# Kernel optimization log

Measured on AMD Instinct MI355X. Metric: run time of the kernel, lower is better.

The kernel has to match this reference:

```python
import jax, jax.numpy as jnp
import numpy as np

B, T, F, H = 64, 2048, 256, 512


def setup_inputs() -> dict:
    key = jax.random.key(0)
    ks = jax.random.split(key, 8)
    s_ih = 1.0 / np.sqrt(H)
    return {
        "z": jax.random.normal(ks[0], (B, H), dtype=jnp.float32),
        "x": jax.random.normal(ks[1], (B, T, F), dtype=jnp.float32),
        "W_ih": jax.random.uniform(ks[2], (4 * H, F), minval=-s_ih, maxval=s_ih, dtype=jnp.float32),
        "W_hh": jax.random.uniform(ks[3], (4 * H, H), minval=-s_ih, maxval=s_ih, dtype=jnp.float32),
        "b_ih": jax.random.uniform(ks[4], (4 * H,), minval=-s_ih, maxval=s_ih, dtype=jnp.float32),
        "b_hh": jax.random.uniform(ks[5], (4 * H,), minval=-s_ih, maxval=s_ih, dtype=jnp.float32),
        "W_lin": jax.random.uniform(ks[6], (F, H), minval=-s_ih, maxval=s_ih, dtype=jnp.float32),
        "b_lin": jax.random.uniform(ks[7], (F,), minval=-s_ih, maxval=s_ih, dtype=jnp.float32),
    }


def _lstm_decode(z, x, W_ih, W_hh, b_ih, b_hh, W_lin, b_lin):
    # Teacher forcing: cell input at step t is x[:, t]. h0 = z, c0 = 0.
    # Precompute input projections for all timesteps in one GEMM: [T, B, 4H]
    x_t_major = jnp.swapaxes(x, 0, 1)  # [T, B, F]
    x_proj = jnp.einsum("tbf,gf->tbg", x_t_major, W_ih) + (b_ih + b_hh)
    h0 = z
    c0 = jnp.zeros_like(z)

    def step(carry, xp):
        h, c = carry
        gates = xp + h @ W_hh.T  # [B, 4H]
        i, f, g, o = jnp.split(gates, 4, axis=-1)  # PyTorch gate order: i,f,g,o
        i = jax.nn.sigmoid(i)
        f = jax.nn.sigmoid(f)
        g = jnp.tanh(g)
        o = jax.nn.sigmoid(o)
        c_new = f * c + i * g
        h_new = o * jnp.tanh(c_new)
        out_t = h_new @ W_lin.T + b_lin  # [B, F]
        return (h_new, c_new), out_t

    _, outs = jax.lax.scan(step, (h0, c0), x_proj)  # outs: [T, B, F]
    return jnp.swapaxes(outs, 0, 1)  # [B, T, F]


def reference(z, x, W_ih, W_hh, b_ih, b_hh, W_lin, b_lin):
    return _lstm_decode(z, x, W_ih, W_hh, b_ih, b_hh, W_lin, b_lin)
```

## Files before the change

### kernel.cpp

```cpp
#include <hip/hip_runtime.h>
#include <hip/hip_bf16.h>

#define B_   64
#define T_   2048
#define F_   256
#define H_   512
#define NWG  64

typedef __attribute__((ext_vector_type(8))) short bfrag;
typedef __attribute__((ext_vector_type(4))) int   int4v;
typedef __attribute__((ext_vector_type(4))) float f32x4;
typedef __attribute__((ext_vector_type(4))) float float4_t;

__device__ __forceinline__ float fsig(float x)  { return 1.0f / (1.0f + __expf(-x)); }
__device__ __forceinline__ float ftanh(float x) { return 2.0f / (1.0f + __expf(-2.0f * x)) - 1.0f; }

__device__ __forceinline__ short f2bf(float f) {
  __hip_bfloat16 h = __float2bfloat16(f);
  return __builtin_bit_cast(short, h);
}

__device__ __forceinline__ int4v gload16_cc(const void* p) {
  int4v r;
  asm volatile("global_load_dwordx4 %0, %1, off sc0 sc1" : "=v"(r) : "v"(p));
  return r;
}
__device__ __forceinline__ int gload_flag(const void* p) {
  int r;
  asm volatile("global_load_dword %0, %1, off sc0 sc1\n\ts_waitcnt vmcnt(0)"
               : "=v"(r) : "v"(p) : "memory");
  return r;
}
__device__ __forceinline__ void gstore4_cc(void* p, unsigned int d) {
  asm volatile("global_store_dword %0, %1, off sc0 sc1" :: "v"(p), "v"(d));
}
__device__ __forceinline__ void vm_drain() {
  asm volatile("s_waitcnt vmcnt(0)" ::: "memory");
  __builtin_amdgcn_sched_barrier(0);
}

__global__ void lstm_init(const float* __restrict__ z, __hip_bfloat16* __restrict__ hb0,
                          int* __restrict__ wgdone) {
  int i = blockIdx.x * blockDim.x + threadIdx.x;
  if (i < NWG) wgdone[i] = 0;
  for (int idx = i; idx < B_ * H_; idx += gridDim.x * blockDim.x)
    hb0[idx] = __float2bfloat16(z[idx]);
}

__global__ void __launch_bounds__(256, 1)
lstm_persist(const float* __restrict__ x,
             const float* __restrict__ Wih,  const float* __restrict__ Whh,
             const float* __restrict__ bih,  const float* __restrict__ bhh,
             const float* __restrict__ Wlin, const float* __restrict__ blin,
             float* __restrict__ out,
             __hip_bfloat16* __restrict__ hb0, __hip_bfloat16* __restrict__ hb1,
             int* __restrict__ wgdone)
{
  const int g   = blockIdx.x;
  const int tid = threadIdx.x;
  const int wv  = tid >> 6;
  const int l   = tid & 63;
  const int l16 = l & 15;
  const int lk  = (l >> 4) << 3;

  bfrag BW[2][24];
  #pragma unroll
  for (int nt = 0; nt < 2; ++nt) {
    const int n   = nt * 16 + l16;
    const int row = (n >> 3) * H_ + g * 8 + (n & 7);
    #pragma unroll
    for (int kt = 0; kt < 24; ++kt) {
      const float* src = (kt < 8) ? (Wih + (size_t)row * F_ + kt * 32 + lk)
                                  : (Whh + (size_t)row * H_ + (kt - 8) * 32 + lk);
      bfrag w;
      #pragma unroll
      for (int e = 0; e < 8; ++e) w[e] = f2bf(src[e]);
      BW[nt][kt] = w;
    }
  }
  bfrag BL[16];
  {
    const bool v  = (l16 < 4);
    const int col = g * 4 + (l16 & 3);
    #pragma unroll
    for (int kt = 0; kt < 16; ++kt) {
      bfrag w;
      #pragma unroll
      for (int e = 0; e < 8; ++e)
        w[e] = v ? f2bf(Wlin[(size_t)col * H_ + kt * 32 + lk + e]) : (short)0;
      BL[kt] = w;
    }
  }
  float bs0 = 0.f, bs1 = 0.f, bs2 = 0.f, bs3 = 0.f, blc = 0.f;
  if (l16 < 8) {
    const int c0 = g * 8 + l16;
    bs0 = bih[c0]          + bhh[c0];
    bs1 = bih[H_ + c0]     + bhh[H_ + c0];
    bs2 = bih[2 * H_ + c0] + bhh[2 * H_ + c0];
    bs3 = bih[3 * H_ + c0] + bhh[3 * H_ + c0];
  }
  if (l16 < 4) blc = blin[g * 4 + l16];

  float c4[4] = {0.f, 0.f, 0.f, 0.f};

  const int am     = wv * 16 + l16;
  const int dmBase = wv * 16 + ((l >> 4) << 2);

  auto xpart = [&](int t, f32x4& a0, f32x4& a1) {
    const float* xrow = x + ((size_t)am * T_ + t) * F_ + lk;
    #pragma unroll
    for (int kt = 0; kt < 8; ++kt) {
      float4_t xa = *(const float4_t*)(xrow + kt * 32);
      float4_t xb = *(const float4_t*)(xrow + kt * 32 + 4);
      bfrag a;
      #pragma unroll
      for (int e = 0; e < 4; ++e) { a[e] = f2bf(xa[e]); a[4 + e] = f2bf(xb[e]); }
      a0 = __builtin_amdgcn_mfma_f32_16x16x32_bf16(a, BW[0][kt], a0, 0, 0, 0);
      a1 = __builtin_amdgcn_mfma_f32_16x16x32_bf16(a, BW[1][kt], a1, 0, 0, 0);
    }
  };

  f32x4 xp0 = {0.f, 0.f, 0.f, 0.f}, xp1 = {0.f, 0.f, 0.f, 0.f};
  xpart(0, xp0, xp1);

  for (int t = 0; t < T_; ++t) {
    if (t > 0) {
      while (true) {
        int v = gload_flag(&wgdone[l]);
        if (__all(v >= t)) break;
        __builtin_amdgcn_s_sleep(1);
      }
      __builtin_amdgcn_sched_barrier(0);
    }

    const __hip_bfloat16* hcur = (t & 1) ? hb1 : hb0;
    __hip_bfloat16*       hnxt = (t & 1) ? hb0 : hb1;

    int4v hv[16];
    const char* hbase = (const char*)hcur + ((size_t)am * H_ + lk) * 2;
    #pragma unroll
    for (int kt = 0; kt < 16; ++kt)
      hv[kt] = gload16_cc(hbase + (size_t)kt * 64);
    vm_drain();

    f32x4 acc0 = xp0, acc1 = xp1;
    #pragma unroll
    for (int kt = 0; kt < 16; ++kt) {
      bfrag ha = __builtin_bit_cast(bfrag, hv[kt]);
      acc0 = __builtin_amdgcn_mfma_f32_16x16x32_bf16(ha, BW[0][8 + kt], acc0, 0, 0, 0);
      acc1 = __builtin_amdgcn_mfma_f32_16x16x32_bf16(ha, BW[1][8 + kt], acc1, 0, 0, 0);
    }

    unsigned int* hst32 = (unsigned int*)hnxt;
    #pragma unroll
    for (int r = 0; r < 4; ++r) {
      float fvx = __shfl_xor(acc0[r], 8);
      float ovx = __shfl_xor(acc1[r], 8);
      float hn = 0.f;
      if (l16 < 8) {
        float iv = fsig(acc0[r] + bs0);
        float fv = fsig(fvx + bs1);
        float gv = ftanh(acc1[r] + bs2);
        float ov = fsig(ovx + bs3);
        float cn = fv * c4[r] + iv * gv;
        c4[r] = cn;
        hn = ov * ftanh(cn);
      }
      int hb16 = (int)(unsigned short)f2bf(hn);
      int pu   = __shfl_xor(hb16, 1);
      if ((l16 < 8) && ((l16 & 1) == 0)) {
        unsigned int packed = ((unsigned)hb16 & 0xffffu) | ((unsigned)pu << 16);
        gstore4_cc(&hst32[((size_t)(dmBase + r) * H_ + g * 8 + l16) >> 1], packed);
      }
    }

    vm_drain();
    __syncthreads();
    if (tid == 0)
      gstore4_cc(&wgdone[g], (unsigned int)(t + 1));

    if (t > 0) {
      f32x4 oacc = {blc, blc, blc, blc};
      #pragma unroll
      for (int kt = 0; kt < 16; ++kt) {
        bfrag ha = __builtin_bit_cast(bfrag, hv[kt]);
        oacc = __builtin_amdgcn_mfma_f32_16x16x32_bf16(ha, BL[kt], oacc, 0, 0, 0);
      }
      if (l16 < 4) {
        #pragma unroll
        for (int r = 0; r < 4; ++r)
          out[(size_t)(dmBase + r) * T_ * F_ + (size_t)(t - 1) * F_ + g * 4 + l16] = oacc[r];
      }
    }
    xp0 = (f32x4){0.f, 0.f, 0.f, 0.f};
    xp1 = (f32x4){0.f, 0.f, 0.f, 0.f};
    if (t + 1 < T_) xpart(t + 1, xp0, xp1);
  }

  {
    while (true) {
      int v = gload_flag(&wgdone[l]);
      if (__all(v >= T_)) break;
      __builtin_amdgcn_s_sleep(1);
    }
    __builtin_amdgcn_sched_barrier(0);

    int4v hv[16];
    const char* hbase = (const char*)hb0 + ((size_t)am * H_ + lk) * 2;
    #pragma unroll
    for (int kt = 0; kt < 16; ++kt)
      hv[kt] = gload16_cc(hbase + (size_t)kt * 64);
    vm_drain();

    f32x4 oacc = {blc, blc, blc, blc};
    #pragma unroll
    for (int kt = 0; kt < 16; ++kt) {
      bfrag ha = __builtin_bit_cast(bfrag, hv[kt]);
      oacc = __builtin_amdgcn_mfma_f32_16x16x32_bf16(ha, BL[kt], oacc, 0, 0, 0);
    }
    if (l16 < 4) {
      #pragma unroll
      for (int r = 0; r < 4; ++r)
        out[(size_t)(dmBase + r) * T_ * F_ + (size_t)(T_ - 1) * F_ + g * 4 + l16] = oacc[r];
    }
  }
}

extern "C" void kernel_launch(void* const* d_in, const int* in_sizes, int n_in,
                              void* d_out, int out_size, void* d_ws, size_t ws_size,
                              hipStream_t stream) {
  const float* z    = (const float*)d_in[0];
  const float* x    = (const float*)d_in[1];
  const float* Wih  = (const float*)d_in[2];
  const float* Whh  = (const float*)d_in[3];
  const float* bih  = (const float*)d_in[4];
  const float* bhh  = (const float*)d_in[5];
  const float* Wlin = (const float*)d_in[6];
  const float* blin = (const float*)d_in[7];
  float* out = (float*)d_out;

  __hip_bfloat16* hb0 = (__hip_bfloat16*)d_ws;
  __hip_bfloat16* hb1 = hb0 + B_ * H_;
  int* wgdone = (int*)((char*)d_ws + (size_t)2 * B_ * H_ * sizeof(__hip_bfloat16));

  lstm_init<<<64, 256, 0, stream>>>(z, hb0, wgdone);
  lstm_persist<<<NWG, 256, 0, stream>>>(x, Wih, Whh, bih, bhh, Wlin, blin, out,
                                        hb0, hb1, wgdone);
}
```

Before: 15.39 ms.

## Coalesce h loads via swizzled LDS staging and vectorize h stores

Each wave now loads its 16 rows of the bf16 hidden state as contiguous full-row 16-byte chunks and stages them through an XOR-swizzled LDS buffer, then reads the MFMA A-fragments back from LDS. The h writes are gathered across lanes with shuffles into a single 16-byte store per row instead of four 4-byte stores. This targets poorly coalesced cache-coherent global traffic on the per-step critical path. It adds LDS writes and reads plus shuffles to every timestep.

```diff
diff --git a/kernel.cpp b/kernel.cpp
--- a/kernel.cpp
+++ b/kernel.cpp
@@ -34,8 +34,15 @@
 __device__ __forceinline__ void gstore4_cc(void* p, unsigned int d) {
   asm volatile("global_store_dword %0, %1, off sc0 sc1" :: "v"(p), "v"(d));
 }
+__device__ __forceinline__ void gstore16_cc(void* p, int4v d) {
+  asm volatile("global_store_dwordx4 %0, %1, off sc0 sc1" :: "v"(p), "v"(d));
+}
 __device__ __forceinline__ void vm_drain() {
   asm volatile("s_waitcnt vmcnt(0)" ::: "memory");
+  __builtin_amdgcn_sched_barrier(0);
+}
+__device__ __forceinline__ void lds_drain() {
+  asm volatile("s_waitcnt lgkmcnt(0)" ::: "memory");
   __builtin_amdgcn_sched_barrier(0);
 }
 
@@ -56,12 +63,15 @@
              __hip_bfloat16* __restrict__ hb0, __hip_bfloat16* __restrict__ hb1,
              int* __restrict__ wgdone)
 {
+  __shared__ int4v sm[4096];
+
   const int g   = blockIdx.x;
   const int tid = threadIdx.x;
   const int wv  = tid >> 6;
   const int l   = tid & 63;
   const int l16 = l & 15;
-  const int lk  = (l >> 4) << 3;
+  const int q   = l >> 4;
+  const int lk  = q << 3;
 
   bfrag BW[2][24];
   #pragma unroll
@@ -104,7 +114,11 @@
   float c4[4] = {0.f, 0.f, 0.f, 0.f};
 
   const int am     = wv * 16 + l16;
-  const int dmBase = wv * 16 + ((l >> 4) << 2);
+  const int dmBase = wv * 16 + (q << 2);
+
+  auto fragIdx = [&](int kt) {
+    return wv * 1024 + l16 * 64 + ((kt * 4 + q) ^ (l16 & 7));
+  };
 
   auto xpart = [&](int t, f32x4& a0, f32x4& a1) {
     const float* xrow = x + ((size_t)am * T_ + t) * F_ + lk;
@@ -137,21 +151,25 @@
     __hip_bfloat16*       hnxt = (t & 1) ? hb0 : hb1;
 
     int4v hv[16];
-    const char* hbase = (const char*)hcur + ((size_t)am * H_ + lk) * 2;
-    #pragma unroll
-    for (int kt = 0; kt < 16; ++kt)
-      hv[kt] = gload16_cc(hbase + (size_t)kt * 64);
+    const char* hbase = (const char*)hcur + (size_t)(wv * 16) * (H_ * 2) + l * 16;
+    #pragma unroll
+    for (int j = 0; j < 16; ++j)
+      hv[j] = gload16_cc(hbase + (size_t)j * (H_ * 2));
     vm_drain();
 
+    #pragma unroll
+    for (int j = 0; j < 16; ++j)
+      sm[wv * 1024 + j * 64 + (l ^ (j & 7))] = hv[j];
+    lds_drain();
+
     f32x4 acc0 = xp0, acc1 = xp1;
     #pragma unroll
     for (int kt = 0; kt < 16; ++kt) {
-      bfrag ha = __builtin_bit_cast(bfrag, hv[kt]);
+      bfrag ha = __builtin_bit_cast(bfrag, sm[fragIdx(kt)]);
       acc0 = __builtin_amdgcn_mfma_f32_16x16x32_bf16(ha, BW[0][8 + kt], acc0, 0, 0, 0);
       acc1 = __builtin_amdgcn_mfma_f32_16x16x32_bf16(ha, BW[1][8 + kt], acc1, 0, 0, 0);
     }
 
-    unsigned int* hst32 = (unsigned int*)hnxt;
     #pragma unroll
     for (int r = 0; r < 4; ++r) {
       float fvx = __shfl_xor(acc0[r], 8);
@@ -168,9 +186,15 @@
       }
       int hb16 = (int)(unsigned short)f2bf(hn);
       int pu   = __shfl_xor(hb16, 1);
-      if ((l16 < 8) && ((l16 & 1) == 0)) {
-        unsigned int packed = ((unsigned)hb16 & 0xffffu) | ((unsigned)pu << 16);
-        gstore4_cc(&hst32[((size_t)(dmBase + r) * H_ + g * 8 + l16) >> 1], packed);
+      unsigned int packed = ((unsigned)hb16 & 0xffffu) | ((unsigned)pu << 16);
+      const int base = l & 48;
+      unsigned int p0 = __shfl(packed, base + 0);
+      unsigned int p1 = __shfl(packed, base + 2);
+      unsigned int p2 = __shfl(packed, base + 4);
+      unsigned int p3 = __shfl(packed, base + 6);
+      if (l16 == 0) {
+        int4v v4 = {(int)p0, (int)p1, (int)p2, (int)p3};
+        gstore16_cc((char*)hnxt + (size_t)(dmBase + r) * (H_ * 2) + g * 16, v4);
       }
     }
 
@@ -183,7 +207,7 @@
       f32x4 oacc = {blc, blc, blc, blc};
       #pragma unroll
       for (int kt = 0; kt < 16; ++kt) {
-        bfrag ha = __builtin_bit_cast(bfrag, hv[kt]);
+        bfrag ha = __builtin_bit_cast(bfrag, sm[fragIdx(kt)]);
         oacc = __builtin_amdgcn_mfma_f32_16x16x32_bf16(ha, BL[kt], oacc, 0, 0, 0);
       }
       if (l16 < 4) {
@@ -206,16 +230,20 @@
     __builtin_amdgcn_sched_barrier(0);
 
     int4v hv[16];
-    const char* hbase = (const char*)hb0 + ((size_t)am * H_ + lk) * 2;
-    #pragma unroll
-    for (int kt = 0; kt < 16; ++kt)
-      hv[kt] = gload16_cc(hbase + (size_t)kt * 64);
+    const char* hbase = (const char*)hb0 + (size_t)(wv * 16) * (H_ * 2) + l * 16;
+    #pragma unroll
+    for (int j = 0; j < 16; ++j)
+      hv[j] = gload16_cc(hbase + (size_t)j * (H_ * 2));
     vm_drain();
+    #pragma unroll
+    for (int j = 0; j < 16; ++j)
+      sm[wv * 1024 + j * 64 + (l ^ (j & 7))] = hv[j];
+    lds_drain();
 
     f32x4 oacc = {blc, blc, blc, blc};
     #pragma unroll
     for (int kt = 0; kt < 16; ++kt) {
-      bfrag ha = __builtin_bit_cast(bfrag, hv[kt]);
+      bfrag ha = __builtin_bit_cast(bfrag, sm[fragIdx(kt)]);
       oacc = __builtin_amdgcn_mfma_f32_16x16x32_bf16(ha, BL[kt], oacc, 0, 0, 0);
     }
     if (l16 < 4) {
```

After: 15.55 ms. Within noise of the previous version (+1.0%).
